# Kernel tuning notes

Hardware: AMD Instinct MI355X
Metric: run time of the kernel (lower is better)

The kernel has to match this reference:

```python
import jax, jax.numpy as jnp
import numpy as np

DT = 0.001       # integration timestep
ALPHA = 20.0     # super-spike surrogate slope
VTH = 1.0        # spike threshold (v_leak = v_reset = 0 per norse defaults)
B, T, NIN, H, NOUT = 128, 512, 12, 512, 4

@jax.custom_vjp
def spike(x):
    # norse heaviside with super-spike surrogate gradient
    return (x > 0).astype(x.dtype)

def _spike_fwd(x):
    return (x > 0).astype(x.dtype), x

def _spike_bwd(x, g):
    return (g / (ALPHA * jnp.abs(x) + 1.0) ** 2,)

spike.defvjp(_spike_fwd, _spike_bwd)


def setup_inputs() -> dict:
    key = jax.random.key(0)
    ks = jax.random.split(key, 5)
    x = jax.random.normal(ks[0], (B, T, NIN), dtype=jnp.float32)
    w_in = jax.random.normal(ks[1], (H, NIN), dtype=jnp.float32) / np.sqrt(NIN)
    w_l1_in = jax.random.normal(ks[2], (H, H), dtype=jnp.float32) / np.sqrt(H)
    w_l1_rec = jax.random.normal(ks[3], (H, H), dtype=jnp.float32) / np.sqrt(H)
    w_out = jax.random.normal(ks[4], (NOUT, H), dtype=jnp.float32) / np.sqrt(H)
    return {
        'x': x,
        'w_in': w_in,
        'w_l1_in': w_l1_in,
        'w_l1_rec': w_l1_rec,
        'w_out': w_out,
        'tau_syn_enc': jnp.full((1, H), 0.1, dtype=jnp.float32),
        'tau_mem_enc': jnp.full((1, H), 0.05, dtype=jnp.float32),
        'tau_syn_l1': jnp.full((1, H), 0.1, dtype=jnp.float32),
        'tau_mem_l1': jnp.full((1, H), 0.05, dtype=jnp.float32),
        'tau_syn_out': jnp.asarray(0.5, dtype=jnp.float32),
        'tau_mem_out': jnp.asarray(0.5, dtype=jnp.float32),
    }


def _snn_forward(x, w_in, w_l1_in, w_l1_rec, w_out,
                 tau_syn_enc, tau_mem_enc, tau_syn_l1, tau_mem_l1,
                 tau_syn_out, tau_mem_out):
    # taus are used as *_inv rates and clamped to [0,1] each forward pass
    ts_enc = jnp.clip(tau_syn_enc, 0.0, 1.0)
    tm_enc = jnp.clip(tau_mem_enc, 0.0, 1.0)
    ts_l1 = jnp.clip(tau_syn_l1, 0.0, 1.0)
    tm_l1 = jnp.clip(tau_mem_l1, 0.0, 1.0)
    ts_out = jnp.clip(tau_syn_out, 0.0, 1.0)
    tm_out = jnp.clip(tau_mem_out, 0.0, 1.0)

    batch = x.shape[0]
    xT = jnp.transpose(x, (1, 0, 2))  # [T, B, NIN]

    z0 = jnp.zeros((batch, w_in.shape[0]), dtype=x.dtype)
    vo0 = jnp.zeros((batch, w_out.shape[0]), dtype=x.dtype)
    carry0 = (z0, z0, z0, z0, z0, vo0, vo0)  # senc_v, senc_i, s1_z, s1_v, s1_i, so_v, so_i

    def step(carry, x_t):
        senc_v, senc_i, s1_z, s1_v, s1_i, so_v, so_i = carry
        cur = x_t @ w_in.T  # fc_input (no bias)
        # LIFCell (feed-forward) encode: norse lif_feed_forward_step
        v_dec = senc_v + DT * tm_enc * (-senc_v + senc_i)
        i_dec = senc_i - DT * ts_enc * senc_i
        z_enc = spike(v_dec - VTH)
        senc_v = (1.0 - z_enc) * v_dec  # v_reset = 0
        senc_i = i_dec + cur
        # LIFRecurrentCell l1: norse lif_step with input+recurrent weights
        v1_dec = s1_v + DT * tm_l1 * (-s1_v + s1_i)
        i1_dec = s1_i - DT * ts_l1 * s1_i
        z1 = spike(v1_dec - VTH)
        s1_v = (1.0 - z1) * v1_dec
        s1_i = i1_dec + z_enc @ w_l1_in.T + s1_z @ w_l1_rec.T
        s1_z = z1
        # with_delay=False: z_rec = z_rec_next = z1
        out_in = z1 @ w_out.T  # fc_output (no bias)
        # LICell: norse li_step (returns v_new)
        so_v = so_v + DT * tm_out * (-so_v + so_i)
        so_i = so_i - DT * ts_out * so_i + out_in
        return (senc_v, senc_i, s1_z, s1_v, s1_i, so_v, so_i), so_v

    _, voltages = jax.lax.scan(step, carry0, xT)
    return voltages  # [T, B, NOUT]


def reference(x, w_in, w_l1_in, w_l1_rec, w_out,
              tau_syn_enc, tau_mem_enc, tau_syn_l1, tau_mem_l1,
              tau_syn_out, tau_mem_out):
    return _snn_forward(x, w_in, w_l1_in, w_l1_rec, w_out,
                        tau_syn_enc, tau_mem_enc, tau_syn_l1, tau_mem_l1,
                        tau_syn_out, tau_mem_out)
```

## Files before the change

### kernel.cpp

```cpp
#include <hip/hip_runtime.h>

#define B_ 128
#define T_ 512
#define NIN_ 12
#define H_ 512
#define NOUT_ 4
#define DT_ 0.001f

typedef unsigned long long ull;

__device__ __align__(16) float g_W1t[H_ * H_];
__device__ __align__(16) float g_WRt[H_ * H_];
__device__ __align__(16) ull g_masks[B_ * T_ * 8];
__device__ __align__(16) ull g_flags[B_ * 8 * 8];
__device__ unsigned g_tstar[B_];

__device__ __forceinline__ float clamp01(float v) { return fminf(fmaxf(v, 0.0f), 1.0f); }

__global__ void transpose_pair(const float* __restrict__ a, const float* __restrict__ bsrc,
                               float* __restrict__ out) {
  const int gtid = (((blockIdx.z * gridDim.y + blockIdx.y) * gridDim.x + blockIdx.x) * 256)
                   + threadIdx.y * 32 + threadIdx.x;
  if (gtid < (T_ * B_ * NOUT_) / 4) {
    float4 z; z.x = 0.f; z.y = 0.f; z.z = 0.f; z.w = 0.f;
    ((float4*)out)[gtid] = z;
  }
  if (gtid < B_) g_tstar[gtid] = T_;

  __shared__ float tile[32][33];
  const float* src = blockIdx.z ? bsrc : a;
  float* dst = blockIdx.z ? g_WRt : g_W1t;
  const int bx = blockIdx.x * 32, by = blockIdx.y * 32;
  const int tx = threadIdx.x, ty = threadIdx.y;
#pragma unroll
  for (int k = 0; k < 32; k += 8)
    tile[ty + k][tx] = src[(size_t)(by + ty + k) * H_ + bx + tx];
  __syncthreads();
#pragma unroll
  for (int k = 0; k < 32; k += 8)
    dst[(size_t)(bx + ty + k) * H_ + by + tx] = tile[tx][ty + k];
}

__global__ __launch_bounds__(256, 1) void snn_phase1(
    const float* __restrict__ x, const float* __restrict__ w_in,
    const float* __restrict__ tse, const float* __restrict__ tme) {
  const int b = blockIdx.x;
  const int g = blockIdx.y;
  const int w = threadIdx.x >> 6;
  const int j = threadIdx.x & 63;
  const int s = g * 4 + w;
  const int n = (j << 3) + s;

  __shared__ float4 xs[(T_ + 4) * 3];
  const float4* xg = (const float4*)(x + (size_t)b * T_ * NIN_);
  for (int i = threadIdx.x; i < T_ * 3; i += 256) xs[i] = xg[i];

  float win[NIN_];
#pragma unroll
  for (int i = 0; i < NIN_; ++i) win[i] = w_in[n * NIN_ + i];
  const float ae = DT_ * clamp01(tme[n]);
  const float be = DT_ * clamp01(tse[n]);
  float ev = 0.f, ei = 0.f;
  ull* mout = g_masks + (size_t)b * T_ * 8 + s;
  ull* gfo = g_flags + (size_t)b * 64 + s;
  ull flag = 0;
  __syncthreads();

  float4 A0 = xs[0], A1 = xs[1],  A2 = xs[2];
  float4 B0 = xs[3], B1 = xs[4],  B2 = xs[5];
  float4 C0 = xs[6], C1 = xs[7],  C2 = xs[8];
  float4 D0 = xs[9], D1 = xs[10], D2 = xs[11];

  auto STEP = [&](float4& xa, float4& xb, float4& xc, int t) {
    float c0 = 0.f, c1 = 0.f, c2 = 0.f, c3 = 0.f;
    c0 = fmaf(xa.x, win[0], c0); c1 = fmaf(xa.y, win[1], c1);
    c2 = fmaf(xa.z, win[2], c2); c3 = fmaf(xa.w, win[3], c3);
    c0 = fmaf(xb.x, win[4], c0); c1 = fmaf(xb.y, win[5], c1);
    c2 = fmaf(xb.z, win[6], c2); c3 = fmaf(xb.w, win[7], c3);
    c0 = fmaf(xc.x, win[8], c0); c1 = fmaf(xc.y, win[9], c1);
    c2 = fmaf(xc.z, win[10], c2); c3 = fmaf(xc.w, win[11], c3);
    const float c = (c0 + c1) + (c2 + c3);
    const int pf = (t + 4) * 3;
    xa = xs[pf]; xb = xs[pf + 1]; xc = xs[pf + 2];
    const float vdec = fmaf(ae, ei - ev, ev);
    const bool ze = vdec > 1.0f;
    const ull m = __ballot(ze);
    ev = ze ? 0.0f : vdec;
    ei = fmaf(-be, ei, ei) + c;
    if (j == 0) mout[(size_t)t * 8] = m;
    flag |= (m ? 1ull : 0ull) << (t & 63);
    if ((t & 63) == 63) { if (j == 0) gfo[(size_t)(t >> 6) * 8] = flag; flag = 0; }
  };

  for (int t = 0; t < T_; t += 4) {
    STEP(A0, A1, A2, t);
    STEP(B0, B1, B2, t + 1);
    STEP(C0, C1, C2, t + 2);
    STEP(D0, D1, D2, t + 3);
  }
}

__global__ __launch_bounds__(256, 1) void snn_spec(
    const float* __restrict__ ts1, const float* __restrict__ tm1) {
  const int b = blockIdx.x;
  const int n = blockIdx.y * 256 + threadIdx.x;
  const float a1 = DT_ * clamp01(tm1[n]);
  const float b1 = DT_ * clamp01(ts1[n]);
  float v1 = 0.f, i1 = 0.f;
  unsigned tstar = 0xFFFFFFFFu;

  const ull* __restrict__ mb = g_masks + (size_t)b * T_ * 8;
  const ull* __restrict__ fb = g_flags + (size_t)b * 64;

  for (int win = 0; win < 8; ++win) {
    const ulonglong2* fp = (const ulonglong2*)(fb + (size_t)win * 8);
    const ulonglong2 p0 = fp[0], p1 = fp[1], p2 = fp[2], p3 = fp[3];
    const ull wf = p0.x | p0.y | p1.x | p1.y | p2.x | p2.y | p3.x | p3.y;
    const int t0 = win * 64;
#pragma unroll 4
    for (int tc = 0; tc < 64; ++tc) {
      const int t = t0 + tc;
      const float vd = fmaf(a1, i1 - v1, v1);
      tstar = (vd > 1.0f) ? min(tstar, (unsigned)t) : tstar;
      v1 = vd;
      float acc = 0.f;
      if ((wf >> tc) & 1) {
        const ulonglong2* mp = (const ulonglong2*)(mb + (size_t)t * 8);
        const ulonglong2 q0 = mp[0], q1 = mp[1], q2 = mp[2], q3 = mp[3];
        const ull cm8[8] = {q0.x, q0.y, q1.x, q1.y, q2.x, q2.y, q3.x, q3.y};
#pragma unroll
        for (int s = 0; s < 8; ++s) {
          ull m = cm8[s];
          while (m) {
            const int jj = __builtin_ctzll(m); m &= m - 1;
            acc += g_W1t[(size_t)((jj << 3) + s) * H_ + n];
          }
        }
      }
      i1 = fmaf(-b1, i1, i1) + acc;
    }
  }
  if (tstar != 0xFFFFFFFFu) atomicMin(&g_tstar[b], tstar);
}

__global__ __launch_bounds__(64, 1) void snn_fixup(
    const float* __restrict__ w_out,
    const float* __restrict__ ts1, const float* __restrict__ tm1,
    const float* __restrict__ tso, const float* __restrict__ tmo,
    float* __restrict__ out) {
  const int b = blockIdx.x;
  if (g_tstar[b] >= T_) return;
  const int l = threadIdx.x;

  float a1[8], b1[8], v1[8], i1[8];
#pragma unroll
  for (int s = 0; s < 8; ++s) {
    const int n = (l << 3) + s;
    a1[s] = DT_ * clamp01(tm1[n]);
    b1[s] = DT_ * clamp01(ts1[n]);
    v1[s] = 0.f; i1[s] = 0.f;
  }
  const float ao = DT_ * clamp01(tmo[0]);
  const float bo = DT_ * clamp01(tso[0]);
  float sov = 0.f, soi = 0.f;
  const float* wo = w_out + (l & 3) * H_;

  ull zp[8];
#pragma unroll
  for (int s = 0; s < 8; ++s) zp[s] = 0ULL;

  const ull* __restrict__ mb = g_masks + (size_t)b * T_ * 8;
  const ull* __restrict__ fb = g_flags + (size_t)b * 64;

  ull wf;
  {
    const ulonglong2* fp = (const ulonglong2*)fb;
    const ulonglong2 p0 = fp[0], p1 = fp[1], p2 = fp[2], p3 = fp[3];
    wf = p0.x | p0.y | p1.x | p1.y | p2.x | p2.y | p3.x | p3.y;
  }

  for (int win = 0; win < 8; ++win) {
    ulonglong2 f0 = {0,0}, f1 = {0,0}, f2 = {0,0}, f3 = {0,0};
    if (win < 7) {
      const ulonglong2* fp = (const ulonglong2*)(fb + (size_t)(win + 1) * 8);
      f0 = fp[0]; f1 = fp[1]; f2 = fp[2]; f3 = fp[3];
    }
    const int t0 = win * 64;
#pragma unroll 1
    for (int tc = 0; tc < 64; ++tc) {
      const int t = t0 + tc;
      ull mz[8];
#pragma unroll
      for (int s = 0; s < 8; ++s) {
        const float vd = v1[s] + a1[s] * (i1[s] - v1[s]);
        const float id = i1[s] - b1[s] * i1[s];
        const bool z = (vd - 1.0f) > 0.0f;
        v1[s] = z ? 0.0f : vd;
        i1[s] = id;
        mz[s] = __ballot(z);
      }
      if ((wf >> tc) & 1) {
        const ulonglong2* mp = (const ulonglong2*)(mb + (size_t)t * 8);
        const ulonglong2 q0 = mp[0], q1 = mp[1], q2 = mp[2], q3 = mp[3];
        const ull cm8[8] = {q0.x, q0.y, q1.x, q1.y, q2.x, q2.y, q3.x, q3.y};
#pragma unroll
        for (int s = 0; s < 8; ++s) {
          ull m = cm8[s];
          while (m) {
            const int jj = __builtin_ctzll(m); m &= m - 1;
            const float4* r = (const float4*)(g_W1t + (size_t)((jj << 3) + s) * H_);
            const float4 ra = r[2 * l], rb = r[2 * l + 1];
            i1[0] += ra.x; i1[1] += ra.y; i1[2] += ra.z; i1[3] += ra.w;
            i1[4] += rb.x; i1[5] += rb.y; i1[6] += rb.z; i1[7] += rb.w;
          }
        }
      }
      if (zp[0] | zp[1] | zp[2] | zp[3] | zp[4] | zp[5] | zp[6] | zp[7]) {
#pragma unroll
        for (int s = 0; s < 8; ++s) {
          ull m = zp[s];
          while (m) {
            const int jj = __builtin_ctzll(m); m &= m - 1;
            const float4* r = (const float4*)(g_WRt + (size_t)((jj << 3) + s) * H_);
            const float4 ra = r[2 * l], rb = r[2 * l + 1];
            i1[0] += ra.x; i1[1] += ra.y; i1[2] += ra.z; i1[3] += ra.w;
            i1[4] += rb.x; i1[5] += rb.y; i1[6] += rb.z; i1[7] += rb.w;
          }
        }
      }
      float oin = 0.f;
      if (mz[0] | mz[1] | mz[2] | mz[3] | mz[4] | mz[5] | mz[6] | mz[7]) {
#pragma unroll
        for (int s = 0; s < 8; ++s) {
          ull m = mz[s];
          while (m) {
            const int jj = __builtin_ctzll(m); m &= m - 1;
            oin += wo[(jj << 3) + s];
          }
        }
      }
      sov = sov + ao * (soi - sov);
      soi = soi - bo * soi + oin;
      if (l < NOUT_) out[((size_t)t * B_ + b) * NOUT_ + l] = sov;
#pragma unroll
      for (int s = 0; s < 8; ++s) zp[s] = mz[s];
    }
    wf = f0.x | f0.y | f1.x | f1.y | f2.x | f2.y | f3.x | f3.y;
  }
}

extern "C" void kernel_launch(void* const* d_in, const int* in_sizes, int n_in,
                              void* d_out, int out_size, void* d_ws, size_t ws_size,
                              hipStream_t stream) {
  const float* x    = (const float*)d_in[0];
  const float* w_in = (const float*)d_in[1];
  const float* w1   = (const float*)d_in[2];
  const float* wrec = (const float*)d_in[3];
  const float* wout = (const float*)d_in[4];
  const float* tse  = (const float*)d_in[5];
  const float* tme  = (const float*)d_in[6];
  const float* ts1  = (const float*)d_in[7];
  const float* tm1  = (const float*)d_in[8];
  const float* tso  = (const float*)d_in[9];
  const float* tmo  = (const float*)d_in[10];
  float* out = (float*)d_out;

  transpose_pair<<<dim3(16, 16, 2), dim3(32, 8), 0, stream>>>(w1, wrec, out);
  snn_phase1<<<dim3(B_, 2), dim3(256), 0, stream>>>(x, w_in, tse, tme);
  snn_spec<<<dim3(B_, 2), dim3(256), 0, stream>>>(ts1, tm1);
  snn_fixup<<<dim3(B_), dim3(64), 0, stream>>>(wout, ts1, tm1, tso, tmo, out);
}
```

Baseline: 167.0 us.

## Double-buffer encoder inputs and prefetch next spike mask in speculative layer pass

In phase1, the per-step shared-memory input prefetch becomes a double-buffered register scheme of 8-step groups, with sched barriers so LDS loads for the next half-group are issued ahead of compute. In the speculative layer-1 pass, the per-timestep loop becomes an event-driven walk over active timesteps. It prefetches the next active timestep's masks while gathering up to four weight columns in parallel, and runs a tight decay-only loop between events. This targets serialized memory latency on the recurrent critical path, at the cost of more registers and an overflow path that changes summation order.

```diff
diff --git a/kernel.cpp b/kernel.cpp
--- a/kernel.cpp
+++ b/kernel.cpp
@@ -51,7 +51,7 @@
   const int s = g * 4 + w;
   const int n = (j << 3) + s;
 
-  __shared__ float4 xs[(T_ + 4) * 3];
+  __shared__ float4 xs[(T_ + 8) * 3];
   const float4* xg = (const float4*)(x + (size_t)b * T_ * NIN_);
   for (int i = threadIdx.x; i < T_ * 3; i += 256) xs[i] = xg[i];
 
@@ -66,38 +66,52 @@
   ull flag = 0;
   __syncthreads();
 
-  float4 A0 = xs[0], A1 = xs[1],  A2 = xs[2];
-  float4 B0 = xs[3], B1 = xs[4],  B2 = xs[5];
-  float4 C0 = xs[6], C1 = xs[7],  C2 = xs[8];
-  float4 D0 = xs[9], D1 = xs[10], D2 = xs[11];
-
-  auto STEP = [&](float4& xa, float4& xb, float4& xc, int t) {
-    float c0 = 0.f, c1 = 0.f, c2 = 0.f, c3 = 0.f;
-    c0 = fmaf(xa.x, win[0], c0); c1 = fmaf(xa.y, win[1], c1);
-    c2 = fmaf(xa.z, win[2], c2); c3 = fmaf(xa.w, win[3], c3);
-    c0 = fmaf(xb.x, win[4], c0); c1 = fmaf(xb.y, win[5], c1);
-    c2 = fmaf(xb.z, win[6], c2); c3 = fmaf(xb.w, win[7], c3);
-    c0 = fmaf(xc.x, win[8], c0); c1 = fmaf(xc.y, win[9], c1);
-    c2 = fmaf(xc.z, win[10], c2); c3 = fmaf(xc.w, win[11], c3);
-    const float c = (c0 + c1) + (c2 + c3);
-    const int pf = (t + 4) * 3;
-    xa = xs[pf]; xb = xs[pf + 1]; xc = xs[pf + 2];
-    const float vdec = fmaf(ae, ei - ev, ev);
-    const bool ze = vdec > 1.0f;
-    const ull m = __ballot(ze);
-    ev = ze ? 0.0f : vdec;
-    ei = fmaf(-be, ei, ei) + c;
-    if (j == 0) mout[(size_t)t * 8] = m;
-    flag |= (m ? 1ull : 0ull) << (t & 63);
-    if ((t & 63) == 63) { if (j == 0) gfo[(size_t)(t >> 6) * 8] = flag; flag = 0; }
-  };
-
-  for (int t = 0; t < T_; t += 4) {
-    STEP(A0, A1, A2, t);
-    STEP(B0, B1, B2, t + 1);
-    STEP(C0, C1, C2, t + 2);
-    STEP(D0, D1, D2, t + 3);
-  }
+  float4 bufA[12], bufB[12];
+#pragma unroll
+  for (int q = 0; q < 12; ++q) bufA[q] = xs[q];
+
+#define PSTEP(BUF, SLOT, TT)                                                  \
+  {                                                                           \
+    const float4 xa = BUF[(SLOT)*3], xb = BUF[(SLOT)*3 + 1], xc = BUF[(SLOT)*3 + 2]; \
+    float c0 = 0.f, c1 = 0.f, c2 = 0.f, c3 = 0.f;                             \
+    c0 = fmaf(xa.x, win[0], c0);  c1 = fmaf(xa.y, win[1], c1);                \
+    c2 = fmaf(xa.z, win[2], c2);  c3 = fmaf(xa.w, win[3], c3);                \
+    c0 = fmaf(xb.x, win[4], c0);  c1 = fmaf(xb.y, win[5], c1);                \
+    c2 = fmaf(xb.z, win[6], c2);  c3 = fmaf(xb.w, win[7], c3);                \
+    c0 = fmaf(xc.x, win[8], c0);  c1 = fmaf(xc.y, win[9], c1);                \
+    c2 = fmaf(xc.z, win[10], c2); c3 = fmaf(xc.w, win[11], c3);               \
+    const float c = (c0 + c1) + (c2 + c3);                                    \
+    const float vdec = fmaf(ae, ei - ev, ev);                                 \
+    const bool ze = vdec > 1.0f;                                              \
+    const ull m = __ballot(ze);                                               \
+    ev = ze ? 0.0f : vdec;                                                    \
+    ei = fmaf(-be, ei, ei) + c;                                               \
+    if (j == 0) mout[(size_t)(TT) * 8] = m;                                   \
+    flag |= (m ? 1ull : 0ull) << ((TT) & 63);                                 \
+    if (((TT) & 63) == 63) {                                                  \
+      if (j == 0) gfo[(size_t)((TT) >> 6) * 8] = flag;                        \
+      flag = 0;                                                               \
+    }                                                                         \
+  }
+
+#pragma unroll 1
+  for (int tg = 0; tg < T_; tg += 8) {
+#pragma unroll
+    for (int q = 0; q < 12; ++q) bufB[q] = xs[(tg + 4) * 3 + q];
+    __builtin_amdgcn_sched_barrier(0);
+    PSTEP(bufA, 0, tg);
+    PSTEP(bufA, 1, tg + 1);
+    PSTEP(bufA, 2, tg + 2);
+    PSTEP(bufA, 3, tg + 3);
+#pragma unroll
+    for (int q = 0; q < 12; ++q) bufA[q] = xs[(tg + 8) * 3 + q];
+    __builtin_amdgcn_sched_barrier(0);
+    PSTEP(bufB, 0, tg + 4);
+    PSTEP(bufB, 1, tg + 5);
+    PSTEP(bufB, 2, tg + 6);
+    PSTEP(bufB, 3, tg + 7);
+  }
+#undef PSTEP
 }
 
 __global__ __launch_bounds__(256, 1) void snn_spec(
@@ -112,34 +126,93 @@
   const ull* __restrict__ mb = g_masks + (size_t)b * T_ * 8;
   const ull* __restrict__ fb = g_flags + (size_t)b * 64;
 
-  for (int win = 0; win < 8; ++win) {
-    const ulonglong2* fp = (const ulonglong2*)(fb + (size_t)win * 8);
+  ull wfs[8];
+#pragma unroll
+  for (int w2 = 0; w2 < 8; ++w2) {
+    const ulonglong2* fp = (const ulonglong2*)(fb + (size_t)w2 * 8);
     const ulonglong2 p0 = fp[0], p1 = fp[1], p2 = fp[2], p3 = fp[3];
-    const ull wf = p0.x | p0.y | p1.x | p1.y | p2.x | p2.y | p3.x | p3.y;
-    const int t0 = win * 64;
-#pragma unroll 4
-    for (int tc = 0; tc < 64; ++tc) {
-      const int t = t0 + tc;
-      const float vd = fmaf(a1, i1 - v1, v1);
-      tstar = (vd > 1.0f) ? min(tstar, (unsigned)t) : tstar;
-      v1 = vd;
-      float acc = 0.f;
-      if ((wf >> tc) & 1) {
-        const ulonglong2* mp = (const ulonglong2*)(mb + (size_t)t * 8);
+    wfs[w2] = p0.x | p0.y | p1.x | p1.y | p2.x | p2.y | p3.x | p3.y;
+  }
+
+#define DECAY_TO(TE)                                                \
+  for (; t < (TE); ++t) {                                           \
+    const float vd = fmaf(a1, i1 - v1, v1);                         \
+    if (vd > 1.0f) tstar = min(tstar, (unsigned)t);                 \
+    v1 = vd;                                                        \
+    i1 = fmaf(-b1, i1, i1);                                         \
+  }
+
+  int t = 0;
+#pragma unroll
+  for (int w2 = 0; w2 < 8; ++w2) {
+    ull rem = wfs[w2];
+    const int wend = w2 * 64 + 64;
+    int te = -1;
+    ull cm[8];
+    if (rem) {
+      te = w2 * 64 + __builtin_ctzll(rem);
+      rem &= rem - 1;
+      const ulonglong2* mp = (const ulonglong2*)(mb + (size_t)te * 8);
+      const ulonglong2 q0 = mp[0], q1 = mp[1], q2 = mp[2], q3 = mp[3];
+      cm[0] = q0.x; cm[1] = q0.y; cm[2] = q1.x; cm[3] = q1.y;
+      cm[4] = q2.x; cm[5] = q2.y; cm[6] = q3.x; cm[7] = q3.y;
+    }
+#pragma unroll 1
+    while (te >= 0) {
+      int te2 = -1;
+      ull nm[8] = {0, 0, 0, 0, 0, 0, 0, 0};
+      if (rem) {
+        te2 = w2 * 64 + __builtin_ctzll(rem);
+        rem &= rem - 1;
+        const ulonglong2* mp = (const ulonglong2*)(mb + (size_t)te2 * 8);
         const ulonglong2 q0 = mp[0], q1 = mp[1], q2 = mp[2], q3 = mp[3];
-        const ull cm8[8] = {q0.x, q0.y, q1.x, q1.y, q2.x, q2.y, q3.x, q3.y};
+        nm[0] = q0.x; nm[1] = q0.y; nm[2] = q1.x; nm[3] = q1.y;
+        nm[4] = q2.x; nm[5] = q2.y; nm[6] = q3.x; nm[7] = q3.y;
+      }
+      int h0 = -1, h1 = -1, h2 = -1, h3 = -1, kc = 0;
+#pragma unroll
+      for (int s = 0; s < 8; ++s) {
+        ull m = cm[s];
+        while (m) {
+          const int jj = __builtin_ctzll(m); m &= m - 1;
+          const int hs = (jj << 3) + s;
+          if (kc == 0) h0 = hs; else if (kc == 1) h1 = hs;
+          else if (kc == 2) h2 = hs; else if (kc == 3) h3 = hs;
+          ++kc;
+        }
+      }
+      float q0v = 0.f, q1v = 0.f, q2v = 0.f, q3v = 0.f;
+      if (h0 >= 0) q0v = g_W1t[(size_t)h0 * H_ + n];
+      if (h1 >= 0) q1v = g_W1t[(size_t)h1 * H_ + n];
+      if (h2 >= 0) q2v = g_W1t[(size_t)h2 * H_ + n];
+      if (h3 >= 0) q3v = g_W1t[(size_t)h3 * H_ + n];
+      float ovf = 0.f;
+      if (kc > 4) {
+        int skip = 4;
 #pragma unroll
         for (int s = 0; s < 8; ++s) {
-          ull m = cm8[s];
+          ull m = cm[s];
           while (m) {
             const int jj = __builtin_ctzll(m); m &= m - 1;
-            acc += g_W1t[(size_t)((jj << 3) + s) * H_ + n];
+            if (skip > 0) { --skip; continue; }
+            ovf += g_W1t[(size_t)((jj << 3) + s) * H_ + n];
           }
         }
       }
-      i1 = fmaf(-b1, i1, i1) + acc;
+      DECAY_TO(te);
+      const float vd = fmaf(a1, i1 - v1, v1);
+      if (vd > 1.0f) tstar = min(tstar, (unsigned)te);
+      v1 = vd;
+      i1 = fmaf(-b1, i1, i1) + (((q0v + q1v) + (q2v + q3v)) + ovf);
+      t = te + 1;
+      te = te2;
+#pragma unroll
+      for (int q = 0; q < 8; ++q) cm[q] = nm[q];
     }
-  }
+    DECAY_TO(wend);
+  }
+#undef DECAY_TO
+
   if (tstar != 0xFFFFFFFFu) atomicMin(&g_tstar[b], tstar);
 }
 
```

Result: faster. 152.3 us (-8.8%).
